# Performance work log

Measured on AMD Instinct MI355X. Metric: run time of the kernel, lower is better.

The kernel has to match this reference:

```python
import jax, jax.numpy as jnp
import numpy as np

EMBED_DIM = 1024
HEAD_SIZE = 64
BATCH = 8
SEQ = 2048


def setup_inputs() -> dict:
    key = jax.random.key(0)
    k1, k2, k3, k4 = jax.random.split(key, 4)
    x = jax.random.normal(k1, (BATCH, SEQ, EMBED_DIM), dtype=jnp.float32)
    # Dense(use_bias=False) kernels: [in, out]
    scale = 1.0 / np.sqrt(EMBED_DIM)
    Wq = jax.random.normal(k2, (EMBED_DIM, HEAD_SIZE), dtype=jnp.float32) * scale
    Wk = jax.random.normal(k3, (EMBED_DIM, HEAD_SIZE), dtype=jnp.float32) * scale
    Wv = jax.random.normal(k4, (EMBED_DIM, HEAD_SIZE), dtype=jnp.float32) * scale
    return {"x": x, "Wq": Wq, "Wk": Wk, "Wv": Wv}


def reference(x, Wq, Wk, Wv):
    B, S, E = x.shape
    q = jnp.einsum("bse,eh->bsh", x, Wq)
    k = jnp.einsum("bse,eh->bsh", x, Wk)
    v = jnp.einsum("bse,eh->bsh", x, Wv)
    # scores scaled by embedding_dim**-0.5 (as in the original code)
    w = jnp.einsum("bqh,bkh->bqk", q, k) * (E ** -0.5)
    causal = jnp.tril(jnp.ones((S, S), dtype=bool))  # True on/below diag
    w = jnp.where(causal, w, -jnp.inf)
    w = jax.nn.softmax(w, axis=-1)
    # dropout is identity at inference
    return jnp.einsum("bqk,bkh->bqh", w, v)
```

## Files before the change

kernel.cpp:

```cpp
#include <hip/hip_runtime.h>
#include <hip/hip_bf16.h>


#define BATCH 8
#define SEQ   2048
#define EMB   1024
#define HD    64
#define ROWS  (BATCH*SEQ)
#define NTOT  192

typedef __attribute__((ext_vector_type(8))) short short8;
typedef __attribute__((ext_vector_type(4))) float floatx4;

static __device__ __forceinline__ short f2bf(float f) {
  union { __hip_bfloat16 h; short s; } u;
  u.h = __float2bfloat16(f);
  return u.s;
}

__global__ __launch_bounds__(256) void wt_kernel(
    const float* __restrict__ Wq, const float* __restrict__ Wk,
    const float* __restrict__ Wv, short* __restrict__ Wt) {
  const int i = blockIdx.x * 256 + threadIdx.x;
  const int np = i % NTOT;
  const int c4 = i / NTOT;
  const float* __restrict__ W = (np < 64) ? Wq : ((np < 128) ? Wk : Wv);
  const int n = np & 63;
  short4 o;
  o.x = f2bf(W[(c4 * 4 + 0) * HD + n]);
  o.y = f2bf(W[(c4 * 4 + 1) * HD + n]);
  o.z = f2bf(W[(c4 * 4 + 2) * HD + n]);
  o.w = f2bf(W[(c4 * 4 + 3) * HD + n]);
  *(short4*)(Wt + (size_t)np * EMB + c4 * 4) = o;
}

#define ASTR 40

__global__ __launch_bounds__(256, 2) void proj_kernel(
    const float* __restrict__ x, const short* __restrict__ Wt,
    short* __restrict__ qb, short* __restrict__ kb, short* __restrict__ vtb) {
  __shared__ __align__(16) short As[2][32 * ASTR];

  const int t = threadIdx.x, lane = t & 63, w = t >> 6;
  const int lo = lane & 15, quad = lane >> 4;
  const int m0 = blockIdx.x * 32;

  const int srow = t >> 3, sc4 = t & 7;
  const float* __restrict__ xs = x + (size_t)(m0 + srow) * EMB + sc4 * 4;

  const short* __restrict__ wb = Wt + (size_t)(w * 3 * 16 + lo) * EMB + quad * 8;

  floatx4 acc[2][3];
#pragma unroll
  for (int mf = 0; mf < 2; ++mf)
#pragma unroll
    for (int j = 0; j < 3; ++j) acc[mf][j] = (floatx4){0.f, 0.f, 0.f, 0.f};

  {
    const float4 xv = *(const float4*)(xs);
    *(short4*)(&As[0][srow * ASTR + sc4 * 4]) =
        make_short4(f2bf(xv.x), f2bf(xv.y), f2bf(xv.z), f2bf(xv.w));
  }
  short8 b0 = *(const short8*)(wb);
  short8 b1 = *(const short8*)(wb + (size_t)16 * EMB);
  short8 b2 = *(const short8*)(wb + (size_t)32 * EMB);

  for (int ks = 0; ks < 32; ++ks) {
    const int buf = ks & 1;
    __syncthreads();

    float4 xn;
    short8 nb0, nb1, nb2;
    if (ks < 31) {
      const int ko = (ks + 1) * 32;
      xn = *(const float4*)(xs + ko);
      nb0 = *(const short8*)(wb + ko);
      nb1 = *(const short8*)(wb + ko + (size_t)16 * EMB);
      nb2 = *(const short8*)(wb + ko + (size_t)32 * EMB);
    }

    const short8 af0 = *(const short8*)(&As[buf][(lo) * ASTR + quad * 8]);
    const short8 af1 = *(const short8*)(&As[buf][(16 + lo) * ASTR + quad * 8]);

    acc[0][0] = __builtin_amdgcn_mfma_f32_16x16x32_bf16(af0, b0, acc[0][0], 0, 0, 0);
    acc[1][0] = __builtin_amdgcn_mfma_f32_16x16x32_bf16(af1, b0, acc[1][0], 0, 0, 0);
    acc[0][1] = __builtin_amdgcn_mfma_f32_16x16x32_bf16(af0, b1, acc[0][1], 0, 0, 0);
    acc[1][1] = __builtin_amdgcn_mfma_f32_16x16x32_bf16(af1, b1, acc[1][1], 0, 0, 0);
    acc[0][2] = __builtin_amdgcn_mfma_f32_16x16x32_bf16(af0, b2, acc[0][2], 0, 0, 0);
    acc[1][2] = __builtin_amdgcn_mfma_f32_16x16x32_bf16(af1, b2, acc[1][2], 0, 0, 0);

    if (ks < 31) {
      *(short4*)(&As[buf ^ 1][srow * ASTR + sc4 * 4]) =
          make_short4(f2bf(xn.x), f2bf(xn.y), f2bf(xn.z), f2bf(xn.w));
      b0 = nb0; b1 = nb1; b2 = nb2;
    }
  }

  const int bb = m0 >> 11;
  const int sbase = (m0 & (SEQ - 1)) + quad * 4;
#pragma unroll
  for (int mf = 0; mf < 2; ++mf) {
    const int rowb = m0 + mf * 16 + quad * 4;
#pragma unroll
    for (int j = 0; j < 3; ++j) {
      const int nt = w * 3 + j;
      const floatx4 v = acc[mf][j];
      if (nt < 4) {
#pragma unroll
        for (int r = 0; r < 4; ++r)
          qb[(size_t)(rowb + r) * HD + nt * 16 + lo] = f2bf(v[r] * 0.03125f);
      } else if (nt < 8) {
#pragma unroll
        for (int r = 0; r < 4; ++r)
          kb[(size_t)(rowb + r) * HD + (nt - 4) * 16 + lo] = f2bf(v[r]);
      } else {
        const int col = (nt - 8) * 16 + lo;
        short4 sv = make_short4(f2bf(v[0]), f2bf(v[1]), f2bf(v[2]), f2bf(v[3]));
        *(short4*)(vtb + ((size_t)bb * HD + col) * SEQ + sbase + mf * 16) = sv;
      }
    }
  }
}

#define KSTR 72
#define PSTR 40

__global__ __launch_bounds__(256, 2) void attn_kernel(
    const short* __restrict__ qb, const short* __restrict__ kb,
    const short* __restrict__ vtb, float* __restrict__ out) {
  __shared__ __align__(16) short Ks[2][64 * KSTR];
  __shared__ __align__(16) short Vs[2][64 * KSTR];
  __shared__ __align__(16) short Ps[4][16 * PSTR];
  __shared__ __align__(16) floatx4 Red[2][5][64];

  const int b = blockIdx.y;
  const int bx = blockIdx.x;
  const int qx = (bx & 1) ? (63 - (bx >> 1)) : (bx >> 1);
  const int q0 = qx * 32;
  const int t = threadIdx.x, lane = t & 63, w = t >> 6;
  const int wr = w >> 1, wk = w & 1;
  const int lo = lane & 15, quad = lane >> 4;

  const short* qp = qb + ((size_t)b * SEQ + q0 + wr * 16 + lo) * HD + quad * 8;
  const short8 qf0 = *(const short8*)(qp);
  const short8 qf1 = *(const short8*)(qp + 32);

  const int r0 = t >> 3, c0 = (t & 7) * 8;
  const int r1 = r0 + 32;
  const short* __restrict__ kgb = kb + (size_t)b * SEQ * HD;
  const short* __restrict__ vgb = vtb + (size_t)b * HD * SEQ;

  floatx4 acc[4];
  float lsum[4] = {0.f, 0.f, 0.f, 0.f};
#pragma unroll
  for (int nt = 0; nt < 4; ++nt) acc[nt] = (floatx4){0.f, 0.f, 0.f, 0.f};

  {
    short8 k0v = *(const short8*)(kgb + (size_t)r0 * HD + c0);
    short8 k1v = *(const short8*)(kgb + (size_t)r1 * HD + c0);
    short8 v0v = *(const short8*)(vgb + (size_t)r0 * SEQ + c0);
    short8 v1v = *(const short8*)(vgb + (size_t)r1 * SEQ + c0);
    *(short8*)(&Ks[0][r0 * KSTR + c0]) = k0v;
    *(short8*)(&Ks[0][r1 * KSTR + c0]) = k1v;
    *(short8*)(&Vs[0][r0 * KSTR + c0]) = v0v;
    *(short8*)(&Vs[0][r1 * KSTR + c0]) = v1v;
  }

  const int niter = q0 / 64 + 1;
  for (int it = 0; it < niter; ++it) {
    const int j0 = it * 64;
    const int buf = it & 1;
    __syncthreads();

    short8 kfr[2][2], vfr[4];
#pragma unroll
    for (int n2 = 0; n2 < 2; ++n2) {
      const short* kr = &Ks[buf][(wk * 32 + n2 * 16 + lo) * KSTR + quad * 8];
      kfr[n2][0] = *(const short8*)(kr);
      kfr[n2][1] = *(const short8*)(kr + 32);
    }
#pragma unroll
    for (int nt = 0; nt < 4; ++nt)
      vfr[nt] = *(const short8*)(&Vs[buf][(nt * 16 + lo) * KSTR + wk * 32 + quad * 8]);

    short8 nk0, nk1, nv0, nv1;
    const bool more = (it + 1 < niter);
    if (more) {
      const int jn = j0 + 64;
      nk0 = *(const short8*)(kgb + (size_t)(jn + r0) * HD + c0);
      nk1 = *(const short8*)(kgb + (size_t)(jn + r1) * HD + c0);
      nv0 = *(const short8*)(vgb + (size_t)r0 * SEQ + jn + c0);
      nv1 = *(const short8*)(vgb + (size_t)r1 * SEQ + jn + c0);
    }

    floatx4 s0 = (floatx4){0.f, 0.f, 0.f, 0.f};
    floatx4 s1 = (floatx4){0.f, 0.f, 0.f, 0.f};
    s0 = __builtin_amdgcn_mfma_f32_16x16x32_bf16(qf0, kfr[0][0], s0, 0, 0, 0);
    s0 = __builtin_amdgcn_mfma_f32_16x16x32_bf16(qf1, kfr[0][1], s0, 0, 0, 0);
    s1 = __builtin_amdgcn_mfma_f32_16x16x32_bf16(qf0, kfr[1][0], s1, 0, 0, 0);
    s1 = __builtin_amdgcn_mfma_f32_16x16x32_bf16(qf1, kfr[1][1], s1, 0, 0, 0);

    const bool diag = (j0 + 64 > q0);
    const int rowb = q0 + wr * 16 + quad * 4;
    short* Pw = Ps[w];
#pragma unroll
    for (int r = 0; r < 4; ++r) {
      float e0 = __expf(s0[r]);
      float e1 = __expf(s1[r]);
      if (diag) {
        const int key0 = j0 + wk * 32 + lo;
        e0 = (key0 <= rowb + r) ? e0 : 0.f;
        e1 = (key0 + 16 <= rowb + r) ? e1 : 0.f;
      }
      lsum[r] += e0 + e1;
      Pw[(quad * 4 + r) * PSTR + lo] = f2bf(e0);
      Pw[(quad * 4 + r) * PSTR + 16 + lo] = f2bf(e1);
    }
    const short8 pf = *(const short8*)(&Pw[lo * PSTR + quad * 8]);
#pragma unroll
    for (int nt = 0; nt < 4; ++nt)
      acc[nt] = __builtin_amdgcn_mfma_f32_16x16x32_bf16(pf, vfr[nt], acc[nt], 0, 0, 0);

    if (more) {
      const int nb = buf ^ 1;
      *(short8*)(&Ks[nb][r0 * KSTR + c0]) = nk0;
      *(short8*)(&Ks[nb][r1 * KSTR + c0]) = nk1;
      *(short8*)(&Vs[nb][r0 * KSTR + c0]) = nv0;
      *(short8*)(&Vs[nb][r1 * KSTR + c0]) = nv1;
    }
  }

#pragma unroll
  for (int d = 1; d < 16; d <<= 1) {
#pragma unroll
    for (int r = 0; r < 4; ++r) lsum[r] += __shfl_xor(lsum[r], d);
  }

  if (wk == 1) {
#pragma unroll
    for (int nt = 0; nt < 4; ++nt) Red[wr][nt][lane] = acc[nt];
    Red[wr][4][lane] = (floatx4){lsum[0], lsum[1], lsum[2], lsum[3]};
  }
  __syncthreads();
  if (wk == 0) {
    const floatx4 lp = Red[wr][4][lane];
    const int rowb = q0 + wr * 16 + quad * 4;
#pragma unroll
    for (int nt = 0; nt < 4; ++nt) {
      const floatx4 o = acc[nt] + Red[wr][nt][lane];
#pragma unroll
      for (int r = 0; r < 4; ++r)
        out[((size_t)b * SEQ + rowb + r) * HD + nt * 16 + lo] =
            o[r] / (lsum[r] + lp[r]);
    }
  }
}

extern "C" void kernel_launch(void* const* d_in, const int* in_sizes, int n_in,
                              void* d_out, int out_size, void* d_ws, size_t ws_size,
                              hipStream_t stream) {
  const float* x  = (const float*)d_in[0];
  const float* Wq = (const float*)d_in[1];
  const float* Wk = (const float*)d_in[2];
  const float* Wv = (const float*)d_in[3];
  float* out = (float*)d_out;
  short* ws = (short*)d_ws;
  short* qbp = ws;
  short* kbp = ws + (size_t)ROWS * HD;
  short* vtp = ws + (size_t)2 * ROWS * HD;
  short* Wt  = ws + (size_t)3 * ROWS * HD;

  wt_kernel<<<dim3(NTOT), 256, 0, stream>>>(Wq, Wk, Wv, Wt);
  proj_kernel<<<dim3(ROWS / 32), 256, 0, stream>>>(x, Wt, qbp, kbp, vtp);
  attn_kernel<<<dim3(SEQ / 32, BATCH), 256, 0, stream>>>(qbp, kbp, vtp, out);
}
```

Baseline: 156.5 us.

## Load x fragments directly to registers in projection, dropping LDS staging and barriers

The projection kernel no longer stages x through shared memory with a barrier every k-step. Each wave now loads its own fp32 x fragments straight from global memory into registers and converts them to bf16 in registers. It also prefetches 128-wide K chunks in a double-buffered register scheme. This removes LDS traffic and __syncthreads, but each of the 4 waves now reads the same x rows redundantly (4x global/L2 reads of x) and register pressure rises sharply.

Result: slower. 178.0 us (+13.7%).

```diff
diff --git a/kernel.cpp b/kernel.cpp
--- a/kernel.cpp
+++ b/kernel.cpp
@@ -16,6 +16,13 @@
   union { __hip_bfloat16 h; short s; } u;
   u.h = __float2bfloat16(f);
   return u.s;
+}
+
+static __device__ __forceinline__ short8 pack8(float4 u, float4 v) {
+  short8 r;
+  r[0] = f2bf(u.x); r[1] = f2bf(u.y); r[2] = f2bf(u.z); r[3] = f2bf(u.w);
+  r[4] = f2bf(v.x); r[5] = f2bf(v.y); r[6] = f2bf(v.z); r[7] = f2bf(v.w);
+  return r;
 }
 
 __global__ __launch_bounds__(256) void wt_kernel(
@@ -34,21 +41,16 @@
   *(short4*)(Wt + (size_t)np * EMB + c4 * 4) = o;
 }
 
-#define ASTR 40
-
 __global__ __launch_bounds__(256, 2) void proj_kernel(
     const float* __restrict__ x, const short* __restrict__ Wt,
-    short* __restrict__ qb, short* __restrict__ kb, short* __restrict__ vtb) {
-  __shared__ __align__(16) short As[2][32 * ASTR];
-
+    short* __restrict__ qb, short* __restrict__ kb_, short* __restrict__ vtb) {
   const int t = threadIdx.x, lane = t & 63, w = t >> 6;
   const int lo = lane & 15, quad = lane >> 4;
   const int m0 = blockIdx.x * 32;
 
-  const int srow = t >> 3, sc4 = t & 7;
-  const float* __restrict__ xs = x + (size_t)(m0 + srow) * EMB + sc4 * 4;
-
-  const short* __restrict__ wb = Wt + (size_t)(w * 3 * 16 + lo) * EMB + quad * 8;
+  const float* __restrict__ xr0 = x + (size_t)(m0 + lo) * EMB + quad * 8;
+  const float* __restrict__ xr1 = xr0 + (size_t)16 * EMB;
+  const short* __restrict__ wb = Wt + (size_t)(w * 48 + lo) * EMB + quad * 8;
 
   floatx4 acc[2][3];
 #pragma unroll
@@ -56,43 +58,73 @@
 #pragma unroll
     for (int j = 0; j < 3; ++j) acc[mf][j] = (floatx4){0.f, 0.f, 0.f, 0.f};
 
-  {
-    const float4 xv = *(const float4*)(xs);
-    *(short4*)(&As[0][srow * ASTR + sc4 * 4]) =
-        make_short4(f2bf(xv.x), f2bf(xv.y), f2bf(xv.z), f2bf(xv.w));
-  }
-  short8 b0 = *(const short8*)(wb);
-  short8 b1 = *(const short8*)(wb + (size_t)16 * EMB);
-  short8 b2 = *(const short8*)(wb + (size_t)32 * EMB);
-
-  for (int ks = 0; ks < 32; ++ks) {
-    const int buf = ks & 1;
-    __syncthreads();
-
-    float4 xn;
-    short8 nb0, nb1, nb2;
-    if (ks < 31) {
-      const int ko = (ks + 1) * 32;
-      xn = *(const float4*)(xs + ko);
-      nb0 = *(const short8*)(wb + ko);
-      nb1 = *(const short8*)(wb + ko + (size_t)16 * EMB);
-      nb2 = *(const short8*)(wb + ko + (size_t)32 * EMB);
-    }
-
-    const short8 af0 = *(const short8*)(&As[buf][(lo) * ASTR + quad * 8]);
-    const short8 af1 = *(const short8*)(&As[buf][(16 + lo) * ASTR + quad * 8]);
-
-    acc[0][0] = __builtin_amdgcn_mfma_f32_16x16x32_bf16(af0, b0, acc[0][0], 0, 0, 0);
-    acc[1][0] = __builtin_amdgcn_mfma_f32_16x16x32_bf16(af1, b0, acc[1][0], 0, 0, 0);
-    acc[0][1] = __builtin_amdgcn_mfma_f32_16x16x32_bf16(af0, b1, acc[0][1], 0, 0, 0);
-    acc[1][1] = __builtin_amdgcn_mfma_f32_16x16x32_bf16(af1, b1, acc[1][1], 0, 0, 0);
-    acc[0][2] = __builtin_amdgcn_mfma_f32_16x16x32_bf16(af0, b2, acc[0][2], 0, 0, 0);
-    acc[1][2] = __builtin_amdgcn_mfma_f32_16x16x32_bf16(af1, b2, acc[1][2], 0, 0, 0);
-
-    if (ks < 31) {
-      *(short4*)(&As[buf ^ 1][srow * ASTR + sc4 * 4]) =
-          make_short4(f2bf(xn.x), f2bf(xn.y), f2bf(xn.z), f2bf(xn.w));
-      b0 = nb0; b1 = nb1; b2 = nb2;
+  float4 A0[4][4], A1[4][4];
+  short8 Bc[4][3];
+
+#pragma unroll
+  for (int s = 0; s < 4; ++s) {
+    A0[s][0] = *(const float4*)(xr0 + s * 32);
+    A0[s][1] = *(const float4*)(xr0 + s * 32 + 4);
+    A0[s][2] = *(const float4*)(xr1 + s * 32);
+    A0[s][3] = *(const float4*)(xr1 + s * 32 + 4);
+  }
+
+  for (int kb = 0; kb < 8; kb += 2) {
+    {
+      const int ko = kb * 128;
+#pragma unroll
+      for (int s = 0; s < 4; ++s) {
+        Bc[s][0] = *(const short8*)(wb + ko + s * 32);
+        Bc[s][1] = *(const short8*)(wb + ko + s * 32 + (size_t)16 * EMB);
+        Bc[s][2] = *(const short8*)(wb + ko + s * 32 + (size_t)32 * EMB);
+      }
+#pragma unroll
+      for (int s = 0; s < 4; ++s) {
+        A1[s][0] = *(const float4*)(xr0 + ko + 128 + s * 32);
+        A1[s][1] = *(const float4*)(xr0 + ko + 128 + s * 32 + 4);
+        A1[s][2] = *(const float4*)(xr1 + ko + 128 + s * 32);
+        A1[s][3] = *(const float4*)(xr1 + ko + 128 + s * 32 + 4);
+      }
+#pragma unroll
+      for (int s = 0; s < 4; ++s) {
+        const short8 af0 = pack8(A0[s][0], A0[s][1]);
+        const short8 af1 = pack8(A0[s][2], A0[s][3]);
+        acc[0][0] = __builtin_amdgcn_mfma_f32_16x16x32_bf16(af0, Bc[s][0], acc[0][0], 0, 0, 0);
+        acc[1][0] = __builtin_amdgcn_mfma_f32_16x16x32_bf16(af1, Bc[s][0], acc[1][0], 0, 0, 0);
+        acc[0][1] = __builtin_amdgcn_mfma_f32_16x16x32_bf16(af0, Bc[s][1], acc[0][1], 0, 0, 0);
+        acc[1][1] = __builtin_amdgcn_mfma_f32_16x16x32_bf16(af1, Bc[s][1], acc[1][1], 0, 0, 0);
+        acc[0][2] = __builtin_amdgcn_mfma_f32_16x16x32_bf16(af0, Bc[s][2], acc[0][2], 0, 0, 0);
+        acc[1][2] = __builtin_amdgcn_mfma_f32_16x16x32_bf16(af1, Bc[s][2], acc[1][2], 0, 0, 0);
+      }
+    }
+    {
+      const int ko = kb * 128 + 128;
+#pragma unroll
+      for (int s = 0; s < 4; ++s) {
+        Bc[s][0] = *(const short8*)(wb + ko + s * 32);
+        Bc[s][1] = *(const short8*)(wb + ko + s * 32 + (size_t)16 * EMB);
+        Bc[s][2] = *(const short8*)(wb + ko + s * 32 + (size_t)32 * EMB);
+      }
+      if (kb + 2 < 8) {
+#pragma unroll
+        for (int s = 0; s < 4; ++s) {
+          A0[s][0] = *(const float4*)(xr0 + ko + 128 + s * 32);
+          A0[s][1] = *(const float4*)(xr0 + ko + 128 + s * 32 + 4);
+          A0[s][2] = *(const float4*)(xr1 + ko + 128 + s * 32);
+          A0[s][3] = *(const float4*)(xr1 + ko + 128 + s * 32 + 4);
+        }
+      }
+#pragma unroll
+      for (int s = 0; s < 4; ++s) {
+        const short8 af0 = pack8(A1[s][0], A1[s][1]);
+        const short8 af1 = pack8(A1[s][2], A1[s][3]);
+        acc[0][0] = __builtin_amdgcn_mfma_f32_16x16x32_bf16(af0, Bc[s][0], acc[0][0], 0, 0, 0);
+        acc[1][0] = __builtin_amdgcn_mfma_f32_16x16x32_bf16(af1, Bc[s][0], acc[1][0], 0, 0, 0);
+        acc[0][1] = __builtin_amdgcn_mfma_f32_16x16x32_bf16(af0, Bc[s][1], acc[0][1], 0, 0, 0);
+        acc[1][1] = __builtin_amdgcn_mfma_f32_16x16x32_bf16(af1, Bc[s][1], acc[1][1], 0, 0, 0);
+        acc[0][2] = __builtin_amdgcn_mfma_f32_16x16x32_bf16(af0, Bc[s][2], acc[0][2], 0, 0, 0);
+        acc[1][2] = __builtin_amdgcn_mfma_f32_16x16x32_bf16(af1, Bc[s][2], acc[1][2], 0, 0, 0);
+      }
     }
   }
 
@@ -112,7 +144,7 @@
       } else if (nt < 8) {
 #pragma unroll
         for (int r = 0; r < 4; ++r)
-          kb[(size_t)(rowb + r) * HD + (nt - 4) * 16 + lo] = f2bf(v[r]);
+          kb_[(size_t)(rowb + r) * HD + (nt - 4) * 16 + lo] = f2bf(v[r]);
       } else {
         const int col = (nt - 8) * 16 + lo;
         short4 sv = make_short4(f2bf(v[0]), f2bf(v[1]), f2bf(v[2]), f2bf(v[3]));
```

## Stage projection tiles via global_load_lds with swizzled LDS layout and BK=64

Applied to the files above, without the earlier changes.

The projection kernel now copies raw fp32 x tiles and pre-swizzled bf16 weight tiles straight from global memory into LDS using global_load_lds. Previously it loaded through registers and converted to bf16 before storing to LDS. The K step grows from 32 to 64, and XOR swizzling is used to avoid LDS bank conflicts. The weight prep kernel is changed to write the swizzled per-k-tile layout. The double buffering is removed, so each iteration waits on two barriers with no prefetch overlap, and the fp32-to-bf16 conversion moves to after the LDS read.

After: 145.0 us. 1.08x faster.

```diff
diff --git a/kernel.cpp b/kernel.cpp
--- a/kernel.cpp
+++ b/kernel.cpp
@@ -8,6 +8,8 @@
 #define HD    64
 #define ROWS  (BATCH*SEQ)
 #define NTOT  192
+#define BK    64
+#define NKT   (EMB / BK)
 
 typedef __attribute__((ext_vector_type(8))) short short8;
 typedef __attribute__((ext_vector_type(4))) float floatx4;
@@ -18,37 +20,58 @@
   return u.s;
 }
 
+static __device__ __forceinline__ short8 pack8(float4 u, float4 v) {
+  short8 r;
+  r[0] = f2bf(u.x); r[1] = f2bf(u.y); r[2] = f2bf(u.z); r[3] = f2bf(u.w);
+  r[4] = f2bf(v.x); r[5] = f2bf(v.y); r[6] = f2bf(v.z); r[7] = f2bf(v.w);
+  return r;
+}
+
+static __device__ __forceinline__ void gload_lds16(const void* g, void* l) {
+  __builtin_amdgcn_global_load_lds(
+      (const __attribute__((address_space(1))) unsigned int*)g,
+      (__attribute__((address_space(3))) unsigned int*)l, 16, 0, 0);
+}
+
 __global__ __launch_bounds__(256) void wt_kernel(
     const float* __restrict__ Wq, const float* __restrict__ Wk,
-    const float* __restrict__ Wv, short* __restrict__ Wt) {
-  const int i = blockIdx.x * 256 + threadIdx.x;
-  const int np = i % NTOT;
-  const int c4 = i / NTOT;
+    const float* __restrict__ Wv, short* __restrict__ Wts) {
+  const int id = blockIdx.x * 256 + threadIdx.x;
+  const int kt = id / 1536;
+  const int rem = id - kt * 1536;
+  const int np = rem >> 3;
+  const int s = rem & 7;
   const float* __restrict__ W = (np < 64) ? Wq : ((np < 128) ? Wk : Wv);
   const int n = np & 63;
-  short4 o;
-  o.x = f2bf(W[(c4 * 4 + 0) * HD + n]);
-  o.y = f2bf(W[(c4 * 4 + 1) * HD + n]);
-  o.z = f2bf(W[(c4 * 4 + 2) * HD + n]);
-  o.w = f2bf(W[(c4 * 4 + 3) * HD + n]);
-  *(short4*)(Wt + (size_t)np * EMB + c4 * 4) = o;
-}
-
-#define ASTR 40
+  const int k0 = kt * BK + (s ^ (np & 7)) * 8;
+  short8 o;
+#pragma unroll
+  for (int u = 0; u < 8; ++u) o[u] = f2bf(W[(size_t)(k0 + u) * HD + n]);
+  *(short8*)(Wts + (size_t)id * 8) = o;
+}
 
 __global__ __launch_bounds__(256, 2) void proj_kernel(
-    const float* __restrict__ x, const short* __restrict__ Wt,
-    short* __restrict__ qb, short* __restrict__ kb, short* __restrict__ vtb) {
-  __shared__ __align__(16) short As[2][32 * ASTR];
+    const float* __restrict__ x, const short* __restrict__ Wts,
+    short* __restrict__ qb, short* __restrict__ kb_, short* __restrict__ vtb) {
+  __shared__ __align__(16) float As[32 * 64];
+  __shared__ __align__(16) short Bs[192 * 64];
 
   const int t = threadIdx.x, lane = t & 63, w = t >> 6;
   const int lo = lane & 15, quad = lane >> 4;
+  const int e = lo & 7;
   const int m0 = blockIdx.x * 32;
 
-  const int srow = t >> 3, sc4 = t & 7;
-  const float* __restrict__ xs = x + (size_t)(m0 + srow) * EMB + sc4 * 4;
-
-  const short* __restrict__ wb = Wt + (size_t)(w * 3 * 16 + lo) * EMB + quad * 8;
+  const int cc0 = w * 2, cc1 = cc0 + 1;
+  const int ar0 = cc0 * 4 + (lane >> 4);
+  const int ar1 = cc1 * 4 + (lane >> 4);
+  const int aj = lane & 15;
+  const float* agp0 = x + (size_t)(m0 + ar0) * EMB + ((aj ^ (ar0 & 7)) * 4);
+  const float* agp1 = x + (size_t)(m0 + ar1) * EMB + ((aj ^ (ar1 & 7)) * 4);
+  float* alp0 = As + cc0 * 256;
+  float* alp1 = As + cc1 * 256;
+
+  const short* bgp = Wts + (size_t)(w * 6) * 512 + lane * 8;
+  short* blp = Bs + (w * 6) * 512;
 
   floatx4 acc[2][3];
 #pragma unroll
@@ -56,44 +79,42 @@
 #pragma unroll
     for (int j = 0; j < 3; ++j) acc[mf][j] = (floatx4){0.f, 0.f, 0.f, 0.f};
 
-  {
-    const float4 xv = *(const float4*)(xs);
-    *(short4*)(&As[0][srow * ASTR + sc4 * 4]) =
-        make_short4(f2bf(xv.x), f2bf(xv.y), f2bf(xv.z), f2bf(xv.w));
-  }
-  short8 b0 = *(const short8*)(wb);
-  short8 b1 = *(const short8*)(wb + (size_t)16 * EMB);
-  short8 b2 = *(const short8*)(wb + (size_t)32 * EMB);
-
-  for (int ks = 0; ks < 32; ++ks) {
-    const int buf = ks & 1;
+  for (int kt = 0; kt < NKT; ++kt) {
     __syncthreads();
-
-    float4 xn;
-    short8 nb0, nb1, nb2;
-    if (ks < 31) {
-      const int ko = (ks + 1) * 32;
-      xn = *(const float4*)(xs + ko);
-      nb0 = *(const short8*)(wb + ko);
-      nb1 = *(const short8*)(wb + ko + (size_t)16 * EMB);
-      nb2 = *(const short8*)(wb + ko + (size_t)32 * EMB);
-    }
-
-    const short8 af0 = *(const short8*)(&As[buf][(lo) * ASTR + quad * 8]);
-    const short8 af1 = *(const short8*)(&As[buf][(16 + lo) * ASTR + quad * 8]);
-
-    acc[0][0] = __builtin_amdgcn_mfma_f32_16x16x32_bf16(af0, b0, acc[0][0], 0, 0, 0);
-    acc[1][0] = __builtin_amdgcn_mfma_f32_16x16x32_bf16(af1, b0, acc[1][0], 0, 0, 0);
-    acc[0][1] = __builtin_amdgcn_mfma_f32_16x16x32_bf16(af0, b1, acc[0][1], 0, 0, 0);
-    acc[1][1] = __builtin_amdgcn_mfma_f32_16x16x32_bf16(af1, b1, acc[1][1], 0, 0, 0);
-    acc[0][2] = __builtin_amdgcn_mfma_f32_16x16x32_bf16(af0, b2, acc[0][2], 0, 0, 0);
-    acc[1][2] = __builtin_amdgcn_mfma_f32_16x16x32_bf16(af1, b2, acc[1][2], 0, 0, 0);
-
-    if (ks < 31) {
-      *(short4*)(&As[buf ^ 1][srow * ASTR + sc4 * 4]) =
-          make_short4(f2bf(xn.x), f2bf(xn.y), f2bf(xn.z), f2bf(xn.w));
-      b0 = nb0; b1 = nb1; b2 = nb2;
-    }
+    gload_lds16(agp0 + kt * BK, alp0);
+    gload_lds16(agp1 + kt * BK, alp1);
+    const short* bg = bgp + (size_t)kt * 12288;
+#pragma unroll
+    for (int i = 0; i < 6; ++i)
+      gload_lds16(bg + i * 512, blp + i * 512);
+    __syncthreads();
+
+    short8 af[2][2];
+#pragma unroll
+    for (int mf = 0; mf < 2; ++mf) {
+      const float* Ar = As + (mf * 16 + lo) * 64;
+#pragma unroll
+      for (int ks = 0; ks < 2; ++ks) {
+        const float4 f0 = *(const float4*)(Ar + (((8 * ks + 2 * quad) ^ e) << 2));
+        const float4 f1 = *(const float4*)(Ar + (((8 * ks + 2 * quad + 1) ^ e) << 2));
+        af[mf][ks] = pack8(f0, f1);
+      }
+    }
+    short8 bf[3][2];
+#pragma unroll
+    for (int j = 0; j < 3; ++j) {
+      const short* Br = Bs + ((w * 3 + j) * 16 + lo) * 64;
+#pragma unroll
+      for (int ks = 0; ks < 2; ++ks)
+        bf[j][ks] = *(const short8*)(Br + (((4 * ks + quad) ^ e) << 3));
+    }
+#pragma unroll
+    for (int ks = 0; ks < 2; ++ks)
+#pragma unroll
+      for (int j = 0; j < 3; ++j) {
+        acc[0][j] = __builtin_amdgcn_mfma_f32_16x16x32_bf16(af[0][ks], bf[j][ks], acc[0][j], 0, 0, 0);
+        acc[1][j] = __builtin_amdgcn_mfma_f32_16x16x32_bf16(af[1][ks], bf[j][ks], acc[1][j], 0, 0, 0);
+      }
   }
 
   const int bb = m0 >> 11;
@@ -112,7 +133,7 @@
       } else if (nt < 8) {
 #pragma unroll
         for (int r = 0; r < 4; ++r)
-          kb[(size_t)(rowb + r) * HD + (nt - 4) * 16 + lo] = f2bf(v[r]);
+          kb_[(size_t)(rowb + r) * HD + (nt - 4) * 16 + lo] = f2bf(v[r]);
       } else {
         const int col = (nt - 8) * 16 + lo;
         short4 sv = make_short4(f2bf(v[0]), f2bf(v[1]), f2bf(v[2]), f2bf(v[3]));
@@ -268,9 +289,9 @@
   short* qbp = ws;
   short* kbp = ws + (size_t)ROWS * HD;
   short* vtp = ws + (size_t)2 * ROWS * HD;
-  short* Wt  = ws + (size_t)3 * ROWS * HD;
-
-  wt_kernel<<<dim3(NTOT), 256, 0, stream>>>(Wq, Wk, Wv, Wt);
-  proj_kernel<<<dim3(ROWS / 32), 256, 0, stream>>>(x, Wt, qbp, kbp, vtp);
+  short* Wts = ws + (size_t)3 * ROWS * HD;
+
+  wt_kernel<<<dim3(96), 256, 0, stream>>>(Wq, Wk, Wv, Wts);
+  proj_kernel<<<dim3(ROWS / 32), 256, 0, stream>>>(x, Wts, qbp, kbp, vtp);
   attn_kernel<<<dim3(SEQ / 32, BATCH), 256, 0, stream>>>(qbp, kbp, vtp, out);
 }
```
